# Kernel tuning notes

Measured on AMD Instinct MI355X. Metric: run time of the kernel, lower is better.

Reference implementation:

```python
import jax, jax.numpy as jnp
import numpy as np

DECAY = 0.99
EPS = 1e-05


def setup_inputs() -> dict:
    key = jax.random.key(0)
    k1, k2, k3, k4 = jax.random.split(key, 4)
    B, T, D, K = 16, 4096, 128, 1024
    return {
        "z": jax.random.normal(k1, (B, T, D), dtype=jnp.float32),
        "embedding": jax.random.normal(k2, (K, D), dtype=jnp.float32),
        "cluster_size": jax.random.uniform(k3, (K,), dtype=jnp.float32),
        "ema_w": jax.random.normal(k4, (K, D), dtype=jnp.float32),
    }


def reference(z, embedding, cluster_size, ema_w):
    B, T, D = z.shape
    K = embedding.shape[0]
    z_flat = z.reshape(B * T, D)

    # Squared-distance matrix [N, K]: ||z||^2 - 2 z E^T + ||E||^2
    dist = (
        jnp.sum(z_flat * z_flat, axis=1, keepdims=True)
        - 2.0 * (z_flat @ embedding.T)
        + jnp.sum(embedding * embedding, axis=1)
    )
    indices = jnp.argmin(dist, axis=1)  # [N]
    z_q = embedding[indices].reshape(B, T, D)

    # EMA codebook update (training branch); segment_sum == one_hot.T @ z, one_hot.sum(0)
    batch_cluster = jax.ops.segment_sum(
        jnp.ones((B * T,), dtype=z.dtype), indices, num_segments=K
    )
    new_cluster_size = cluster_size * DECAY + (1.0 - DECAY) * batch_cluster
    batch_ema = jax.ops.segment_sum(z_flat, indices, num_segments=K)
    new_ema_w = ema_w * DECAY + (1.0 - DECAY) * batch_ema

    n = jnp.sum(new_cluster_size)
    smoothed = (new_cluster_size + EPS) / (n + K * EPS) * n
    new_embedding = new_ema_w / smoothed[:, None]

    # Commitment loss on OLD codebook vectors (matches torch order of ops)
    loss_vq = jnp.mean(jnp.square(jax.lax.stop_gradient(z_q) - z))
    # Straight-through estimator
    z_q_st = z + jax.lax.stop_gradient(z_q - z)

    return (
        z_q_st,
        indices.reshape(B, T),
        loss_vq,
        new_embedding,
        new_cluster_size,
        new_ema_w,
    )
```

## Files before the change

kernel.cpp:

```cpp
#include <hip/hip_runtime.h>

#define K_CODES 1024
#define D_DIM 128
#define N_ROWS 65536
#define DECAY_F 0.99f
#define OMD_F 0.01f
#define EPS_F 1e-5f

#define EPAD 136
#define CHUNK_CODES 128
#define N_CHUNKS 8
#define CHUNK_USHORT (2 * CHUNK_CODES * EPAD)
#define NT 4
#define SEG_TILE 64

#define WS_CNT     0
#define WS_LOSS    1024
#define WS_BE      1028
#define WS_ZERO_END (1028 + 131072)
#define WS_ENORM   132100
#define WS_SMOOTH  133124
#define WS_CUR     134148
#define WS_FIDX    135172
#define WS_BUCKET  200708
#define WS_SCODE   266244
#define WS_EIMG    331780

typedef __bf16 bf8_t __attribute__((ext_vector_type(8)));
typedef float  f4_t  __attribute__((ext_vector_type(4)));

__device__ inline unsigned short f2bf_bits(float f) {
    __bf16 h = (__bf16)f;
    return __builtin_bit_cast(unsigned short, h);
}
__device__ inline float bf_bits2f(unsigned short u) {
    __bf16 h = __builtin_bit_cast(__bf16, u);
    return (float)h;
}

__device__ inline void gld16(const void* g, void* l) {
    __builtin_amdgcn_global_load_lds(
        (const __attribute__((address_space(1))) void*)g,
        (__attribute__((address_space(3))) void*)l, 16, 0, 0);
}

__global__ void vq_prep(const float* __restrict__ emb, float* __restrict__ enorm,
                        unsigned short* __restrict__ eimg) {
    int t = blockIdx.x * blockDim.x + threadIdx.x;
    int code = t >> 5;
    int q = t & 31;
    float4 v = ((const float4*)(emb + (size_t)code * D_DIM))[q];
    int chunk = code >> 7, c = code & 127;
    size_t hbase = (size_t)chunk * CHUNK_USHORT + (size_t)c * EPAD + q * 4;
    size_t lbase = hbase + (size_t)CHUNK_CODES * EPAD;
    float vv[4] = {v.x, v.y, v.z, v.w};
    ushort4 hi, lo;
    unsigned short* hp = (unsigned short*)&hi;
    unsigned short* lp = (unsigned short*)&lo;
#pragma unroll
    for (int i = 0; i < 4; ++i) {
        unsigned short hb = f2bf_bits(vv[i]);
        hp[i] = hb;
        lp[i] = f2bf_bits(vv[i] - bf_bits2f(hb));
    }
    *(ushort4*)(eimg + hbase) = hi;
    *(ushort4*)(eimg + lbase) = lo;

    float s = v.x * v.x + v.y * v.y + v.z * v.z + v.w * v.w;
#pragma unroll
    for (int o = 1; o < 32; o <<= 1) s += __shfl_xor(s, o, 64);
    if (q == 0) enorm[code] = s;
}

__device__ inline void top2_update(float s, int code, float& s1, int& i1, float& s2, int& i2) {
    bool b1 = s < s1;
    bool b2 = s < s2;
    s2 = b1 ? s1 : (b2 ? s : s2);
    i2 = b1 ? i1 : (b2 ? code : i2);
    s1 = b1 ? s : s1;
    i1 = b1 ? code : i1;
}

__device__ inline void top2_merge(float& s1, int& i1, float& s2, int& i2,
                                  float t1, int j1, float t2, int j2) {
    bool bf = (t1 < s1) || (t1 == s1 && j1 < i1);
    float ns1 = bf ? t1 : s1;  int ni1 = bf ? j1 : i1;
    float ca  = bf ? s1 : t1;  int ia  = bf ? i1 : j1;
    float cb  = bf ? t2 : s2;  int ib  = bf ? j2 : i2;
    bool bs = (ca < cb) || (ca == cb && ia < ib);
    s1 = ns1; i1 = ni1;
    s2 = bs ? ca : cb; i2 = bs ? ia : ib;
}

__global__ __launch_bounds__(256) void vq_score(
    const float* __restrict__ z, const unsigned short* __restrict__ eimg,
    const float* __restrict__ enorm_g, const float* __restrict__ emb,
    float* __restrict__ out_zq, float* __restrict__ out_idx,
    int* __restrict__ cnt, unsigned int* __restrict__ fidx,
    float* __restrict__ loss_acc)
{
    __shared__ __align__(16) unsigned short lds[2][CHUNK_USHORT];
    __shared__ __align__(16) float lds_en[K_CODES];

    const int tid  = threadIdx.x;
    const int wv   = tid >> 6;
    const int lane = tid & 63;
    const int l16  = lane & 15;
    const int quad = lane >> 4;
    const int rowbase = blockIdx.x * 256 + wv * 64;

    ((float4*)lds_en)[tid] = ((const float4*)enorm_g)[tid];

    {
        const char* gs = (const char*)eimg;
        char* ls = (char*)&lds[0][0];
        int wb = wv * 17408;
#pragma unroll
        for (int i = 0; i < 17; ++i)
            gld16(gs + wb + i * 1024 + lane * 16, ls + wb + i * 1024);
    }

    bf8_t zh[NT][4], zl[NT][4];
#pragma unroll
    for (int nt = 0; nt < NT; ++nt) {
        int row = rowbase + nt * 16 + l16;
        const float* zr = z + (size_t)row * D_DIM;
#pragma unroll
        for (int ks = 0; ks < 4; ++ks) {
            const float4* p = (const float4*)(zr + ks * 32 + quad * 8);
            float4 a = p[0], b = p[1];
            float v[8] = {a.x, a.y, a.z, a.w, b.x, b.y, b.z, b.w};
#pragma unroll
            for (int i = 0; i < 8; ++i) {
                __bf16 hh = (__bf16)v[i];
                zh[nt][ks][i] = hh;
                zl[nt][ks][i] = (__bf16)(v[i] - (float)hh);
            }
        }
    }

    float s1[NT], s2[NT];
    int   i1[NT], i2[NT];
#pragma unroll
    for (int nt = 0; nt < NT; ++nt) { s1[nt] = 3.4e38f; s2[nt] = 3.4e38f; i1[nt] = 0; i2[nt] = 0; }

    __syncthreads();

    for (int c = 0; c < N_CHUNKS; ++c) {
        const int cur = c & 1;
        if (c + 1 < N_CHUNKS) {
            const char* gs = (const char*)(eimg + (size_t)(c + 1) * CHUNK_USHORT);
            char* ls = (char*)&lds[1 - cur][0];
            int wb = wv * 17408;
#pragma unroll
            for (int i = 0; i < 17; ++i)
                gld16(gs + wb + i * 1024 + lane * 16, ls + wb + i * 1024);
        }
        const unsigned short* buf = &lds[cur][0];

#pragma unroll
        for (int cg = 0; cg < 4; ++cg) {
            f4_t acc[2][NT];
#pragma unroll
            for (int ct = 0; ct < 2; ++ct)
#pragma unroll
                for (int nt = 0; nt < NT; ++nt) acc[ct][nt] = (f4_t)(0.f);

#pragma unroll
            for (int ks = 0; ks < 4; ++ks) {
                bf8_t ah[2], al[2];
#pragma unroll
                for (int ct = 0; ct < 2; ++ct) {
                    int cl = cg * 32 + ct * 16 + l16;
                    int base = cl * EPAD + ks * 32 + quad * 8;
                    ah[ct] = *(const bf8_t*)&buf[base];
                    al[ct] = *(const bf8_t*)&buf[CHUNK_CODES * EPAD + base];
                }
#pragma unroll
                for (int ct = 0; ct < 2; ++ct)
#pragma unroll
                    for (int nt = 0; nt < NT; ++nt) {
                        acc[ct][nt] = __builtin_amdgcn_mfma_f32_16x16x32_bf16(
                            ah[ct], zh[nt][ks], acc[ct][nt], 0, 0, 0);
                        acc[ct][nt] = __builtin_amdgcn_mfma_f32_16x16x32_bf16(
                            al[ct], zh[nt][ks], acc[ct][nt], 0, 0, 0);
                        acc[ct][nt] = __builtin_amdgcn_mfma_f32_16x16x32_bf16(
                            ah[ct], zl[nt][ks], acc[ct][nt], 0, 0, 0);
                    }
            }

#pragma unroll
            for (int ct = 0; ct < 2; ++ct) {
                int cb = c * 128 + cg * 32 + ct * 16 + quad * 4;
                float4 en4 = *(const float4*)&lds_en[cb];
                float env[4] = {en4.x, en4.y, en4.z, en4.w};
#pragma unroll
                for (int nt = 0; nt < NT; ++nt)
#pragma unroll
                    for (int r = 0; r < 4; ++r) {
                        float s = env[r] - 2.0f * acc[ct][nt][r];
                        top2_update(s, cb + r, s1[nt], i1[nt], s2[nt], i2[nt]);
                    }
            }
        }
        __syncthreads();
    }

#pragma unroll
    for (int off = 16; off <= 32; off <<= 1) {
#pragma unroll
        for (int nt = 0; nt < NT; ++nt) {
            float t1 = __shfl_xor(s1[nt], off, 64);
            int   j1 = __shfl_xor(i1[nt], off, 64);
            float t2 = __shfl_xor(s2[nt], off, 64);
            int   j2 = __shfl_xor(i2[nt], off, 64);
            top2_merge(s1[nt], i1[nt], s2[nt], i2[nt], t1, j1, t2, j2);
        }
    }

    float ls = 0.f;
#pragma unroll
    for (int nt = 0; nt < NT; ++nt) {
        int row = rowbase + nt * 16 + l16;
        int j1 = i1[nt], j2 = i2[nt];

        const float4* zp  = (const float4*)(z   + (size_t)row * D_DIM);
        const float4* e1p = (const float4*)(emb + (size_t)j1  * D_DIM);
        const float4* e2p = (const float4*)(emb + (size_t)j2  * D_DIM);

        float4 zv[8], a1[8], a2[8];
#pragma unroll
        for (int ks = 0; ks < 4; ++ks) {
            int o = ks * 8 + quad * 2;
            zv[ks * 2]     = zp[o];   zv[ks * 2 + 1] = zp[o + 1];
            a1[ks * 2]     = e1p[o];  a1[ks * 2 + 1] = e1p[o + 1];
            a2[ks * 2]     = e2p[o];  a2[ks * 2 + 1] = e2p[o + 1];
        }
        float p1 = 0.f, p2 = 0.f;
#pragma unroll
        for (int i = 0; i < 8; ++i) {
            p1 += zv[i].x * a1[i].x + zv[i].y * a1[i].y + zv[i].z * a1[i].z + zv[i].w * a1[i].w;
            p2 += zv[i].x * a2[i].x + zv[i].y * a2[i].y + zv[i].z * a2[i].z + zv[i].w * a2[i].w;
        }
        p1 += __shfl_xor(p1, 16, 64); p1 += __shfl_xor(p1, 32, 64);
        p2 += __shfl_xor(p2, 16, 64); p2 += __shfl_xor(p2, 32, 64);
        float sc1 = lds_en[j1] - 2.0f * p1;
        float sc2 = lds_en[j2] - 2.0f * p2;
        bool use2 = (sc2 < sc1) || (sc2 == sc1 && j2 < j1);
        int best = use2 ? j2 : j1;

        if (quad == 0) {
            out_idx[row] = (float)best;
            fidx[row] = (unsigned int)best;
            atomicAdd(cnt + best, 1);
        }

        float4* oz = (float4*)(out_zq + (size_t)row * D_DIM);
#pragma unroll
        for (int i = 0; i < 8; ++i) {
            float4 q = use2 ? a2[i] : a1[i];
            float4 zvv = zv[i];
            float4 df = {q.x - zvv.x, q.y - zvv.y, q.z - zvv.z, q.w - zvv.w};
            ls += df.x * df.x + df.y * df.y + df.z * df.z + df.w * df.w;
            float4 o = {zvv.x + df.x, zvv.y + df.y, zvv.z + df.z, zvv.w + df.w};
            oz[(i >> 1) * 8 + quad * 2 + (i & 1)] = o;
        }
    }

#pragma unroll
    for (int off = 32; off > 0; off >>= 1) ls += __shfl_down(ls, off, 64);
    if (lane == 0) atomicAdd(loss_acc, ls);
}

__global__ void vq_scan(const int* __restrict__ cnt, int* __restrict__ cursor)
{
    __shared__ int tmp[K_CODES];
    int k = threadIdx.x;
    int c = cnt[k];
    tmp[k] = c;
    __syncthreads();
    for (int off = 1; off < K_CODES; off <<= 1) {
        int t = (k >= off) ? tmp[k - off] : 0;
        __syncthreads();
        tmp[k] += t;
        __syncthreads();
    }
    cursor[k] = tmp[k] - c;
}

__global__ void vq_scatter(const unsigned int* __restrict__ fidx,
                           int* __restrict__ cursor, unsigned int* __restrict__ bucket,
                           int* __restrict__ scode)
{
    int row = blockIdx.x * blockDim.x + threadIdx.x;
    int k = (int)fidx[row];
    int slot = atomicAdd(cursor + k, 1);
    bucket[slot] = (unsigned int)row;
    scode[slot]  = k;
}

__global__ __launch_bounds__(128) void vq_segsum(
    const float* __restrict__ z, const unsigned int* __restrict__ bucket,
    const int* __restrict__ scode, float* __restrict__ be)
{
    __shared__ int sb[SEG_TILE];
    __shared__ int sc[SEG_TILE];
    const int tid = threadIdx.x;
    const int t0  = blockIdx.x * SEG_TILE;

    if (tid < SEG_TILE) sb[tid] = (int)bucket[t0 + tid];
    else if (tid < 2 * SEG_TILE) sc[tid - SEG_TILE] = scode[t0 + tid - SEG_TILE];
    __syncthreads();

    const int d = tid;
    float acc = 0.f;
    int cur = sc[0];

    for (int i = 0; i < SEG_TILE; i += 8) {
        float v[8];
#pragma unroll
        for (int j = 0; j < 8; ++j)
            v[j] = z[(size_t)sb[i + j] * D_DIM + d];
#pragma unroll
        for (int j = 0; j < 8; ++j) {
            int c = sc[i + j];
            if (c != cur) {
                atomicAdd(be + (size_t)cur * D_DIM + d, acc);
                acc = 0.f;
                cur = c;
            }
            acc += v[j];
        }
    }
    atomicAdd(be + (size_t)cur * D_DIM + d, acc);
}

__global__ void vq_finalize1(const float* __restrict__ cs, const int* __restrict__ cnt,
                             const float* __restrict__ loss_acc,
                             float* __restrict__ out_ncs, float* __restrict__ out_loss,
                             float* __restrict__ smoothed)
{
    __shared__ float red[K_CODES];
    int k = threadIdx.x;
    float ncs = cs[k] * DECAY_F + OMD_F * (float)cnt[k];
    out_ncs[k] = ncs;
    red[k] = ncs;
    __syncthreads();
    for (int s = 512; s > 0; s >>= 1) {
        if (k < s) red[k] += red[k + s];
        __syncthreads();
    }
    float n = red[0];
    smoothed[k] = (ncs + EPS_F) / (n + (float)K_CODES * EPS_F) * n;
    if (k == 0) out_loss[0] = loss_acc[0] / (float)((size_t)N_ROWS * D_DIM);
}

__global__ void vq_finalize2(const float* __restrict__ ema_w, const float* __restrict__ be,
                             const float* __restrict__ smoothed,
                             float* __restrict__ out_emb, float* __restrict__ out_ema)
{
    int i = blockIdx.x * blockDim.x + threadIdx.x;
    float e = ema_w[i] * DECAY_F + OMD_F * be[i];
    out_ema[i] = e;
    out_emb[i] = e / smoothed[i >> 7];
}

extern "C" void kernel_launch(void* const* d_in, const int* in_sizes, int n_in,
                              void* d_out, int out_size, void* d_ws, size_t ws_size,
                              hipStream_t stream) {
    const float* z   = (const float*)d_in[0];
    const float* emb = (const float*)d_in[1];
    const float* cs  = (const float*)d_in[2];
    const float* ema = (const float*)d_in[3];

    float* out    = (float*)d_out;
    float* o_zq   = out;
    float* o_idx  = o_zq + (size_t)N_ROWS * D_DIM;
    float* o_loss = o_idx + N_ROWS;
    float* o_emb  = o_loss + 1;
    float* o_ncs  = o_emb + K_CODES * D_DIM;
    float* o_ema  = o_ncs + K_CODES;

    float* ws = (float*)d_ws;
    int*            cnt      = (int*)(ws + WS_CNT);
    float*          lacc     = ws + WS_LOSS;
    float*          be       = ws + WS_BE;
    float*          enorm    = ws + WS_ENORM;
    float*          smoothed = ws + WS_SMOOTH;
    int*            cursor   = (int*)(ws + WS_CUR);
    unsigned int*   fidx     = (unsigned int*)(ws + WS_FIDX);
    unsigned int*   bucket   = (unsigned int*)(ws + WS_BUCKET);
    int*            scode    = (int*)(ws + WS_SCODE);
    unsigned short* eimg     = (unsigned short*)(ws + WS_EIMG);

    hipMemsetAsync(ws, 0, (size_t)WS_ZERO_END * sizeof(float), stream);
    vq_prep<<<128, 256, 0, stream>>>(emb, enorm, eimg);
    vq_score<<<256, 256, 0, stream>>>(z, eimg, enorm, emb,
                                      o_zq, o_idx, cnt, fidx, lacc);
    vq_scan<<<1, K_CODES, 0, stream>>>(cnt, cursor);
    vq_scatter<<<N_ROWS / 256, 256, 0, stream>>>(fidx, cursor, bucket, scode);
    vq_segsum<<<N_ROWS / SEG_TILE, 128, 0, stream>>>(z, bucket, scode, be);
    vq_finalize1<<<1, K_CODES, 0, stream>>>(cs, cnt, lacc, o_ncs, o_loss, smoothed);
    vq_finalize2<<<K_CODES * D_DIM / 256, 256, 0, stream>>>(ema, be, smoothed, o_emb, o_ema);
}
```

Baseline: 222.9 us.

## Split codebook scoring across two blocks and add candidate-refinement kernel

The scoring kernel now splits the codebook into two halves handled by separate blocks, doubling the grid to 512 and allowing two blocks per CU. Each half writes top-2 candidates to a workspace buffer, and a new decide kernel picks the exact winner among four candidates in fp32 and writes z_q, indices, counts and loss. Double-buffered LDS is replaced with a single buffer and synchronous reloads. The memset is folded into the prep kernel, and scan is merged with finalize1, so fewer launches are needed. The cost is an extra pass over z and a candidate round-trip through memory, plus lost load/compute overlap in scoring.

New measurement: 256.4 us. 15.0% more time.

```diff
diff --git a/kernel.cpp b/kernel.cpp
--- a/kernel.cpp
+++ b/kernel.cpp
@@ -9,9 +9,10 @@
 
 #define EPAD 136
 #define CHUNK_CODES 128
-#define N_CHUNKS 8
 #define CHUNK_USHORT (2 * CHUNK_CODES * EPAD)
 #define NT 4
+#define HALF_CODES 512
+#define HALF_CHUNKS 4
 #define SEG_TILE 64
 
 #define WS_CNT     0
@@ -24,7 +25,8 @@
 #define WS_FIDX    135172
 #define WS_BUCKET  200708
 #define WS_SCODE   266244
-#define WS_EIMG    331780
+#define WS_CAND    331780
+#define WS_EIMG    593924
 
 typedef __bf16 bf8_t __attribute__((ext_vector_type(8)));
 typedef float  f4_t  __attribute__((ext_vector_type(4)));
@@ -44,9 +46,11 @@
         (__attribute__((address_space(3))) void*)l, 16, 0, 0);
 }
 
-__global__ void vq_prep(const float* __restrict__ emb, float* __restrict__ enorm,
-                        unsigned short* __restrict__ eimg) {
+__global__ void vq_prep(const float* __restrict__ emb, float* __restrict__ ws,
+                        float* __restrict__ enorm, unsigned short* __restrict__ eimg) {
     int t = blockIdx.x * blockDim.x + threadIdx.x;
+    for (int i = t; i < WS_ZERO_END; i += 32768) ws[i] = 0.f;
+
     int code = t >> 5;
     int q = t & 31;
     float4 v = ((const float4*)(emb + (size_t)code * D_DIM))[q];
@@ -92,28 +96,28 @@
     s2 = bs ? ca : cb; i2 = bs ? ia : ib;
 }
 
-__global__ __launch_bounds__(256) void vq_score(
+__global__ __launch_bounds__(256, 2) void vq_score(
     const float* __restrict__ z, const unsigned short* __restrict__ eimg,
-    const float* __restrict__ enorm_g, const float* __restrict__ emb,
-    float* __restrict__ out_zq, float* __restrict__ out_idx,
-    int* __restrict__ cnt, unsigned int* __restrict__ fidx,
-    float* __restrict__ loss_acc)
-{
-    __shared__ __align__(16) unsigned short lds[2][CHUNK_USHORT];
-    __shared__ __align__(16) float lds_en[K_CODES];
+    const float* __restrict__ enorm_g, unsigned int* __restrict__ cand)
+{
+    __shared__ __align__(16) unsigned short lds[CHUNK_USHORT];
+    __shared__ __align__(16) float lds_en[HALF_CODES];
 
     const int tid  = threadIdx.x;
     const int wv   = tid >> 6;
     const int lane = tid & 63;
     const int l16  = lane & 15;
     const int quad = lane >> 4;
-    const int rowbase = blockIdx.x * 256 + wv * 64;
-
-    ((float4*)lds_en)[tid] = ((const float4*)enorm_g)[tid];
+    const int half = blockIdx.x & 1;
+    const int rg   = blockIdx.x >> 1;
+    const int rowbase = rg * 256 + wv * 64;
+
+    if (tid < HALF_CODES / 4)
+        ((float4*)lds_en)[tid] = ((const float4*)(enorm_g + half * HALF_CODES))[tid];
 
     {
-        const char* gs = (const char*)eimg;
-        char* ls = (char*)&lds[0][0];
+        const char* gs = (const char*)(eimg + (size_t)(half * HALF_CHUNKS) * CHUNK_USHORT);
+        char* ls = (char*)lds;
         int wb = wv * 17408;
 #pragma unroll
         for (int i = 0; i < 17; ++i)
@@ -146,18 +150,7 @@
 
     __syncthreads();
 
-    for (int c = 0; c < N_CHUNKS; ++c) {
-        const int cur = c & 1;
-        if (c + 1 < N_CHUNKS) {
-            const char* gs = (const char*)(eimg + (size_t)(c + 1) * CHUNK_USHORT);
-            char* ls = (char*)&lds[1 - cur][0];
-            int wb = wv * 17408;
-#pragma unroll
-            for (int i = 0; i < 17; ++i)
-                gld16(gs + wb + i * 1024 + lane * 16, ls + wb + i * 1024);
-        }
-        const unsigned short* buf = &lds[cur][0];
-
+    for (int c = 0; c < HALF_CHUNKS; ++c) {
 #pragma unroll
         for (int cg = 0; cg < 4; ++cg) {
             f4_t acc[2][NT];
@@ -173,8 +166,8 @@
                 for (int ct = 0; ct < 2; ++ct) {
                     int cl = cg * 32 + ct * 16 + l16;
                     int base = cl * EPAD + ks * 32 + quad * 8;
-                    ah[ct] = *(const bf8_t*)&buf[base];
-                    al[ct] = *(const bf8_t*)&buf[CHUNK_CODES * EPAD + base];
+                    ah[ct] = *(const bf8_t*)&lds[base];
+                    al[ct] = *(const bf8_t*)&lds[CHUNK_CODES * EPAD + base];
                 }
 #pragma unroll
                 for (int ct = 0; ct < 2; ++ct)
@@ -191,19 +184,30 @@
 
 #pragma unroll
             for (int ct = 0; ct < 2; ++ct) {
-                int cb = c * 128 + cg * 32 + ct * 16 + quad * 4;
-                float4 en4 = *(const float4*)&lds_en[cb];
+                int lc = c * 128 + cg * 32 + ct * 16 + quad * 4;
+                float4 en4 = *(const float4*)&lds_en[lc];
                 float env[4] = {en4.x, en4.y, en4.z, en4.w};
+                int gc = half * HALF_CODES + lc;
 #pragma unroll
                 for (int nt = 0; nt < NT; ++nt)
 #pragma unroll
                     for (int r = 0; r < 4; ++r) {
                         float s = env[r] - 2.0f * acc[ct][nt][r];
-                        top2_update(s, cb + r, s1[nt], i1[nt], s2[nt], i2[nt]);
+                        top2_update(s, gc + r, s1[nt], i1[nt], s2[nt], i2[nt]);
                     }
             }
         }
         __syncthreads();
+        if (c + 1 < HALF_CHUNKS) {
+            const char* gs = (const char*)(eimg +
+                (size_t)(half * HALF_CHUNKS + c + 1) * CHUNK_USHORT);
+            char* ls = (char*)lds;
+            int wb = wv * 17408;
+#pragma unroll
+            for (int i = 0; i < 17; ++i)
+                gld16(gs + wb + i * 1024 + lane * 16, ls + wb + i * 1024);
+            __syncthreads();
+        }
     }
 
 #pragma unroll
@@ -218,66 +222,90 @@
         }
     }
 
+    if (lane < 16) {
+#pragma unroll
+        for (int nt = 0; nt < NT; ++nt) {
+            int row = rowbase + nt * 16 + l16;
+            uint2 p = {(unsigned int)i1[nt], (unsigned int)i2[nt]};
+            *(uint2*)(cand + (size_t)row * 4 + half * 2) = p;
+        }
+    }
+}
+
+__global__ __launch_bounds__(256) void vq_decide(
+    const float* __restrict__ z, const float* __restrict__ emb,
+    const float* __restrict__ enorm, const unsigned int* __restrict__ cand,
+    float* __restrict__ out_zq, float* __restrict__ out_idx,
+    int* __restrict__ cnt, unsigned int* __restrict__ fidx,
+    float* __restrict__ loss_acc)
+{
+    const int tid  = threadIdx.x;
+    const int half = tid & 1;
+    const int row  = blockIdx.x * 128 + (tid >> 1);
+
+    float4 zr[16];
+    const float4* zp = (const float4*)(z + (size_t)row * D_DIM + half * 64);
+#pragma unroll
+    for (int i = 0; i < 16; ++i) zr[i] = zp[i];
+
+    uint4 cd = *(const uint4*)(cand + (size_t)row * 4);
+    int j[4] = {(int)cd.x, (int)cd.y, (int)cd.z, (int)cd.w};
+
+    float bs = 3.4e38f;
+    int   bi = 0x7fffffff;
+#pragma unroll
+    for (int cidx = 0; cidx < 4; ++cidx) {
+        int jj = j[cidx];
+        const float4* ep = (const float4*)(emb + (size_t)jj * D_DIM + half * 64);
+        float p = 0.f;
+#pragma unroll
+        for (int i = 0; i < 16; ++i) {
+            float4 a = ep[i], zv = zr[i];
+            p += zv.x * a.x + zv.y * a.y + zv.z * a.z + zv.w * a.w;
+        }
+        float d = p + __shfl_xor(p, 1, 64);
+        float s = enorm[jj] - 2.0f * d;
+        if (s < bs || (s == bs && jj < bi)) { bs = s; bi = jj; }
+    }
+    int best = bi;
+
+    if (half == 0) {
+        out_idx[row] = (float)best;
+        fidx[row] = (unsigned int)best;
+        atomicAdd(cnt + best, 1);
+    }
+
+    const float4* eq = (const float4*)(emb + (size_t)best * D_DIM + half * 64);
+    float4* oz = (float4*)(out_zq + (size_t)row * D_DIM + half * 64);
+
     float ls = 0.f;
 #pragma unroll
-    for (int nt = 0; nt < NT; ++nt) {
-        int row = rowbase + nt * 16 + l16;
-        int j1 = i1[nt], j2 = i2[nt];
-
-        const float4* zp  = (const float4*)(z   + (size_t)row * D_DIM);
-        const float4* e1p = (const float4*)(emb + (size_t)j1  * D_DIM);
-        const float4* e2p = (const float4*)(emb + (size_t)j2  * D_DIM);
-
-        float4 zv[8], a1[8], a2[8];
-#pragma unroll
-        for (int ks = 0; ks < 4; ++ks) {
-            int o = ks * 8 + quad * 2;
-            zv[ks * 2]     = zp[o];   zv[ks * 2 + 1] = zp[o + 1];
-            a1[ks * 2]     = e1p[o];  a1[ks * 2 + 1] = e1p[o + 1];
-            a2[ks * 2]     = e2p[o];  a2[ks * 2 + 1] = e2p[o + 1];
-        }
-        float p1 = 0.f, p2 = 0.f;
-#pragma unroll
-        for (int i = 0; i < 8; ++i) {
-            p1 += zv[i].x * a1[i].x + zv[i].y * a1[i].y + zv[i].z * a1[i].z + zv[i].w * a1[i].w;
-            p2 += zv[i].x * a2[i].x + zv[i].y * a2[i].y + zv[i].z * a2[i].z + zv[i].w * a2[i].w;
-        }
-        p1 += __shfl_xor(p1, 16, 64); p1 += __shfl_xor(p1, 32, 64);
-        p2 += __shfl_xor(p2, 16, 64); p2 += __shfl_xor(p2, 32, 64);
-        float sc1 = lds_en[j1] - 2.0f * p1;
-        float sc2 = lds_en[j2] - 2.0f * p2;
-        bool use2 = (sc2 < sc1) || (sc2 == sc1 && j2 < j1);
-        int best = use2 ? j2 : j1;
-
-        if (quad == 0) {
-            out_idx[row] = (float)best;
-            fidx[row] = (unsigned int)best;
-            atomicAdd(cnt + best, 1);
-        }
-
-        float4* oz = (float4*)(out_zq + (size_t)row * D_DIM);
-#pragma unroll
-        for (int i = 0; i < 8; ++i) {
-            float4 q = use2 ? a2[i] : a1[i];
-            float4 zvv = zv[i];
-            float4 df = {q.x - zvv.x, q.y - zvv.y, q.z - zvv.z, q.w - zvv.w};
-            ls += df.x * df.x + df.y * df.y + df.z * df.z + df.w * df.w;
-            float4 o = {zvv.x + df.x, zvv.y + df.y, zvv.z + df.z, zvv.w + df.w};
-            oz[(i >> 1) * 8 + quad * 2 + (i & 1)] = o;
-        }
+    for (int i = 0; i < 16; ++i) {
+        float4 q = eq[i], zv = zr[i];
+        float4 df = {q.x - zv.x, q.y - zv.y, q.z - zv.z, q.w - zv.w};
+        ls += df.x * df.x + df.y * df.y + df.z * df.z + df.w * df.w;
+        float4 o = {zv.x + df.x, zv.y + df.y, zv.z + df.z, zv.w + df.w};
+        oz[i] = o;
     }
 
 #pragma unroll
     for (int off = 32; off > 0; off >>= 1) ls += __shfl_down(ls, off, 64);
-    if (lane == 0) atomicAdd(loss_acc, ls);
-}
-
-__global__ void vq_scan(const int* __restrict__ cnt, int* __restrict__ cursor)
+    if ((tid & 63) == 0) atomicAdd(loss_acc, ls);
+}
+
+__global__ void vq_mid(const float* __restrict__ cs, const int* __restrict__ cnt,
+                       const float* __restrict__ loss_acc,
+                       float* __restrict__ out_ncs, float* __restrict__ out_loss,
+                       float* __restrict__ smoothed, int* __restrict__ cursor)
 {
     __shared__ int tmp[K_CODES];
+    __shared__ float red[K_CODES];
     int k = threadIdx.x;
     int c = cnt[k];
     tmp[k] = c;
+    float ncs = cs[k] * DECAY_F + OMD_F * (float)c;
+    out_ncs[k] = ncs;
+    red[k] = ncs;
     __syncthreads();
     for (int off = 1; off < K_CODES; off <<= 1) {
         int t = (k >= off) ? tmp[k - off] : 0;
@@ -286,6 +314,13 @@
         __syncthreads();
     }
     cursor[k] = tmp[k] - c;
+    for (int s = 512; s > 0; s >>= 1) {
+        if (k < s) red[k] += red[k + s];
+        __syncthreads();
+    }
+    float n = red[0];
+    smoothed[k] = (ncs + EPS_F) / (n + (float)K_CODES * EPS_F) * n;
+    if (k == 0) out_loss[0] = loss_acc[0] / (float)((size_t)N_ROWS * D_DIM);
 }
 
 __global__ void vq_scatter(const unsigned int* __restrict__ fidx,
@@ -319,45 +354,25 @@
     for (int i = 0; i < SEG_TILE; i += 8) {
         float v[8];
 #pragma unroll
-        for (int j = 0; j < 8; ++j)
-            v[j] = z[(size_t)sb[i + j] * D_DIM + d];
-#pragma unroll
-        for (int j = 0; j < 8; ++j) {
-            int c = sc[i + j];
+        for (int jx = 0; jx < 8; ++jx)
+            v[jx] = z[(size_t)sb[i + jx] * D_DIM + d];
+#pragma unroll
+        for (int jx = 0; jx < 8; ++jx) {
+            int c = sc[i + jx];
             if (c != cur) {
                 atomicAdd(be + (size_t)cur * D_DIM + d, acc);
                 acc = 0.f;
                 cur = c;
             }
-            acc += v[j];
+            acc += v[jx];
         }
     }
     atomicAdd(be + (size_t)cur * D_DIM + d, acc);
 }
 
-__global__ void vq_finalize1(const float* __restrict__ cs, const int* __restrict__ cnt,
-                             const float* __restrict__ loss_acc,
-                             float* __restrict__ out_ncs, float* __restrict__ out_loss,
-                             float* __restrict__ smoothed)
-{
-    __shared__ float red[K_CODES];
-    int k = threadIdx.x;
-    float ncs = cs[k] * DECAY_F + OMD_F * (float)cnt[k];
-    out_ncs[k] = ncs;
-    red[k] = ncs;
-    __syncthreads();
-    for (int s = 512; s > 0; s >>= 1) {
-        if (k < s) red[k] += red[k + s];
-        __syncthreads();
-    }
-    float n = red[0];
-    smoothed[k] = (ncs + EPS_F) / (n + (float)K_CODES * EPS_F) * n;
-    if (k == 0) out_loss[0] = loss_acc[0] / (float)((size_t)N_ROWS * D_DIM);
-}
-
-__global__ void vq_finalize2(const float* __restrict__ ema_w, const float* __restrict__ be,
-                             const float* __restrict__ smoothed,
-                             float* __restrict__ out_emb, float* __restrict__ out_ema)
+__global__ void vq_fin2(const float* __restrict__ ema_w, const float* __restrict__ be,
+                        const float* __restrict__ smoothed,
+                        float* __restrict__ out_emb, float* __restrict__ out_ema)
 {
     int i = blockIdx.x * blockDim.x + threadIdx.x;
     float e = ema_w[i] * DECAY_F + OMD_F * be[i];
@@ -391,15 +406,15 @@
     unsigned int*   fidx     = (unsigned int*)(ws + WS_FIDX);
     unsigned int*   bucket   = (unsigned int*)(ws + WS_BUCKET);
     int*            scode    = (int*)(ws + WS_SCODE);
+    unsigned int*   cand     = (unsigned int*)(ws + WS_CAND);
     unsigned short* eimg     = (unsigned short*)(ws + WS_EIMG);
 
-    hipMemsetAsync(ws, 0, (size_t)WS_ZERO_END * sizeof(float), stream);
-    vq_prep<<<128, 256, 0, stream>>>(emb, enorm, eimg);
-    vq_score<<<256, 256, 0, stream>>>(z, eimg, enorm, emb,
-                                      o_zq, o_idx, cnt, fidx, lacc);
-    vq_scan<<<1, K_CODES, 0, stream>>>(cnt, cursor);
+    vq_prep<<<128, 256, 0, stream>>>(emb, ws, enorm, eimg);
+    vq_score<<<512, 256, 0, stream>>>(z, eimg, enorm, cand);
+    vq_decide<<<512, 256, 0, stream>>>(z, emb, enorm, cand,
+                                       o_zq, o_idx, cnt, fidx, lacc);
+    vq_mid<<<1, K_CODES, 0, stream>>>(cs, cnt, lacc, o_ncs, o_loss, smoothed, cursor);
     vq_scatter<<<N_ROWS / 256, 256, 0, stream>>>(fidx, cursor, bucket, scode);
     vq_segsum<<<N_ROWS / SEG_TILE, 128, 0, stream>>>(z, bucket, scode, be);
-    vq_finalize1<<<1, K_CODES, 0, stream>>>(cs, cnt, lacc, o_ncs, o_loss, smoothed);
-    vq_finalize2<<<K_CODES * D_DIM / 256, 256, 0, stream>>>(ema, be, smoothed, o_emb, o_ema);
-}
+    vq_fin2<<<K_CODES * D_DIM / 256, 256, 0, stream>>>(ema, be, smoothed, o_emb, o_ema);
+}
```
